# Kernel tuning notes

Measured on AMD Instinct MI355X. Metric: run time of the kernel, lower is better.

## Reference

```python
import jax, jax.numpy as jnp
import numpy as np

EPS = 0.0  # torch .norm division has no eps; keep exact

def setup_inputs() -> dict:
    key = jax.random.key(0)
    B, T, C = 32, 1024, 768
    x = jax.random.normal(key, (B, T, C), dtype=jnp.float32)
    return {"x": x}

def reference(x) -> jnp.ndarray:
    # Faithful device-side math of Block_ATC.forward -> agglomerative_clustering:
    #   metric = x / ||x||_2 (last dim); scores = metric @ metric^T; dist = 1 - scores
    # The subsequent scipy linkage/fcluster runs on CPU per-batch and its results
    # are discarded in the original code (labels stay zeros, forward returns None),
    # so the cosine-distance matrix is the meaningful computed tensor.
    metric = x / jnp.linalg.norm(x, axis=-1, keepdims=True)  # [B,T,C]
    scores = jnp.einsum('btc,bsc->bts', metric, metric)      # [B,T,T]
    return 1.0 - scores
```

## Files before the change

### kernel.cpp

```cpp
#include <hip/hip_runtime.h>
#include <hip/hip_bf16.h>
#include <stdint.h>
#include <math.h>

#define B_DIM 32
#define T_DIM 1024
#define C_DIM 768
#define NTILE 8
#define NTRI  36
#define KITER (C_DIM / 32)

typedef float f32x4 __attribute__((ext_vector_type(4)));

typedef __attribute__((address_space(1))) void gvoid_t;
typedef __attribute__((address_space(3))) void lvoid_t;

__global__ __launch_bounds__(256) void normalize_rows_fp8(const float* __restrict__ x,
                                                          uint32_t* __restrict__ m) {
    const int row  = blockIdx.x * 4 + (threadIdx.x >> 6);
    const int lane = threadIdx.x & 63;
    const float4* xr = (const float4*)(x + (size_t)row * C_DIM);
    float4 v0 = xr[lane];
    float4 v1 = xr[lane + 64];
    float4 v2 = xr[lane + 128];
    float ss = v0.x*v0.x + v0.y*v0.y + v0.z*v0.z + v0.w*v0.w
             + v1.x*v1.x + v1.y*v1.y + v1.z*v1.z + v1.w*v1.w
             + v2.x*v2.x + v2.y*v2.y + v2.z*v2.z + v2.w*v2.w;
    #pragma unroll
    for (int off = 32; off > 0; off >>= 1)
        ss += __shfl_xor(ss, off, 64);
    const float rs = rsqrtf(ss);
    uint32_t* mr = m + (size_t)row * (C_DIM / 4);
    int p;
    p = __builtin_amdgcn_cvt_pk_fp8_f32(v0.x * rs, v0.y * rs, 0, false);
    p = __builtin_amdgcn_cvt_pk_fp8_f32(v0.z * rs, v0.w * rs, p, true);
    mr[lane] = (uint32_t)p;
    p = __builtin_amdgcn_cvt_pk_fp8_f32(v1.x * rs, v1.y * rs, 0, false);
    p = __builtin_amdgcn_cvt_pk_fp8_f32(v1.z * rs, v1.w * rs, p, true);
    mr[lane + 64] = (uint32_t)p;
    p = __builtin_amdgcn_cvt_pk_fp8_f32(v2.x * rs, v2.y * rs, 0, false);
    p = __builtin_amdgcn_cvt_pk_fp8_f32(v2.z * rs, v2.w * rs, p, true);
    mr[lane + 128] = (uint32_t)p;
}

__global__ __launch_bounds__(256) void gemm_nt_sym_fp8(const uint8_t* __restrict__ M,
                                                       float* __restrict__ out) {
    __shared__ uint8_t As[2][128 * 32];
    __shared__ uint8_t Bs[2][128 * 32];

    const int b   = blockIdx.x & 31;
    const int idx = blockIdx.x >> 5;
    int tj = (int)((sqrtf(8.0f * (float)idx + 1.0f) - 1.0f) * 0.5f);
    if (tj * (tj + 1) / 2 > idx) --tj;
    const int ti = idx - tj * (tj + 1) / 2;

    const int tid  = threadIdx.x;
    const int wave = tid >> 6;
    const int lane = tid & 63;
    const int quad = lane >> 4;
    const int l16  = lane & 15;
    const int wi = wave >> 1;
    const int wj = wave & 1;

    const uint8_t* Mb = M + (size_t)b * T_DIM * C_DIM;

    const int srow = wave * 32 + (lane >> 1);
    const int scol = (lane & 1) * 16;

    const uint8_t* gA = Mb + (size_t)(ti * 128 + srow) * C_DIM + scol;
    const uint8_t* gB = Mb + (size_t)(tj * 128 + srow) * C_DIM + scol;
    const int cbase = wave * 1024;

    f32x4 acc[4][4];
    #pragma unroll
    for (int i = 0; i < 4; ++i)
        #pragma unroll
        for (int j = 0; j < 4; ++j)
            acc[i][j] = (f32x4){0.f, 0.f, 0.f, 0.f};

    __builtin_amdgcn_global_load_lds((gvoid_t*)gA, (lvoid_t*)&As[0][cbase], 16, 0, 0);
    __builtin_amdgcn_global_load_lds((gvoid_t*)gB, (lvoid_t*)&Bs[0][cbase], 16, 0, 0);

    for (int it = 0; it < KITER; ++it) {
        const int cur = it & 1;
        __syncthreads();
        if (it + 1 < KITER) {
            const int k0 = (it + 1) * 32;
            const int nxt = cur ^ 1;
            __builtin_amdgcn_global_load_lds((gvoid_t*)(gA + k0), (lvoid_t*)&As[nxt][cbase], 16, 0, 0);
            __builtin_amdgcn_global_load_lds((gvoid_t*)(gB + k0), (lvoid_t*)&Bs[nxt][cbase], 16, 0, 0);
        }

        long af[4], bfr[4];
        #pragma unroll
        for (int ii = 0; ii < 4; ++ii) {
            af[ii]  = *(const long*)&As[cur][(wi * 64 + ii * 16 + l16) * 32 + quad * 8];
            bfr[ii] = *(const long*)&Bs[cur][(wj * 64 + ii * 16 + l16) * 32 + quad * 8];
        }
        #pragma unroll
        for (int ii = 0; ii < 4; ++ii)
            #pragma unroll
            for (int jj = 0; jj < 4; ++jj)
                acc[ii][jj] = __builtin_amdgcn_mfma_f32_16x16x32_fp8_fp8(af[ii], bfr[jj], acc[ii][jj], 0, 0, 0);
    }

    float* outb = out + (size_t)b * T_DIM * T_DIM;
    #pragma unroll
    for (int ii = 0; ii < 4; ++ii) {
        const int rowbase = ti * 128 + wi * 64 + ii * 16 + quad * 4;
        #pragma unroll
        for (int jj = 0; jj < 4; ++jj) {
            const int col = tj * 128 + wj * 64 + jj * 16 + l16;
            #pragma unroll
            for (int r = 0; r < 4; ++r)
                outb[(size_t)(rowbase + r) * T_DIM + col] = 1.0f - acc[ii][jj][r];
        }
    }
    if (ti != tj) {
        #pragma unroll
        for (int ii = 0; ii < 4; ++ii) {
            const int rowbase = ti * 128 + wi * 64 + ii * 16 + quad * 4;
            #pragma unroll
            for (int jj = 0; jj < 4; ++jj) {
                const int col = tj * 128 + wj * 64 + jj * 16 + l16;
                f32x4 v;
                v[0] = 1.0f - acc[ii][jj][0];
                v[1] = 1.0f - acc[ii][jj][1];
                v[2] = 1.0f - acc[ii][jj][2];
                v[3] = 1.0f - acc[ii][jj][3];
                *(f32x4*)(outb + (size_t)col * T_DIM + rowbase) = v;
            }
        }
    }
}

extern "C" void kernel_launch(void* const* d_in, const int* in_sizes, int n_in,
                              void* d_out, int out_size, void* d_ws, size_t ws_size,
                              hipStream_t stream) {
    const float* x = (const float*)d_in[0];
    float* out = (float*)d_out;
    uint32_t* metric = (uint32_t*)d_ws;

    normalize_rows_fp8<<<dim3((B_DIM * T_DIM) / 4), dim3(256), 0, stream>>>(x, metric);
    gemm_nt_sym_fp8<<<dim3(NTRI * B_DIM), dim3(256), 0, stream>>>((const uint8_t*)metric, out);
}
```

Before: 250.3 us.

## Deepen LDS pipeline to four buffers with vmcnt waits and swizzle LDS layout

Expands the shared-memory staging from double to quad buffering with a prefetch distance of three K-steps. The full __syncthreads is replaced by explicit s_waitcnt vmcnt plus a raw barrier, so loads for later iterations can stay in flight. An XOR swizzle on the 16-byte column halves, keyed by row bit 2, is applied to both the global-to-LDS copy and the LDS fragment reads to reduce bank conflicts. The costs are more LDS per block (which may lower occupancy) and the risk that the hand-counted vmcnt values and the barrier placement leave a race between overwriting a buffer and other waves still reading it.

```diff
diff --git a/kernel.cpp b/kernel.cpp
--- a/kernel.cpp
+++ b/kernel.cpp
@@ -9,6 +9,7 @@
 #define NTILE 8
 #define NTRI  36
 #define KITER (C_DIM / 32)
+#define NBUF  4
 
 typedef float f32x4 __attribute__((ext_vector_type(4)));
 
@@ -45,8 +46,8 @@
 
 __global__ __launch_bounds__(256) void gemm_nt_sym_fp8(const uint8_t* __restrict__ M,
                                                        float* __restrict__ out) {
-    __shared__ uint8_t As[2][128 * 32];
-    __shared__ uint8_t Bs[2][128 * 32];
+    __shared__ uint8_t As[NBUF][128 * 32];
+    __shared__ uint8_t Bs[NBUF][128 * 32];
 
     const int b   = blockIdx.x & 31;
     const int idx = blockIdx.x >> 5;
@@ -65,11 +66,19 @@
     const uint8_t* Mb = M + (size_t)b * T_DIM * C_DIM;
 
     const int srow = wave * 32 + (lane >> 1);
-    const int scol = (lane & 1) * 16;
+    const int scol = ((lane & 1) * 16) ^ ((((srow >> 2) & 1)) << 4);
 
     const uint8_t* gA = Mb + (size_t)(ti * 128 + srow) * C_DIM + scol;
     const uint8_t* gB = Mb + (size_t)(tj * 128 + srow) * C_DIM + scol;
     const int cbase = wave * 1024;
+
+    const int sw = ((l16 >> 2) & 1) << 4;
+    int offA[4], offB[4];
+    #pragma unroll
+    for (int ii = 0; ii < 4; ++ii) {
+        offA[ii] = (wi * 64 + ii * 16 + l16) * 32 + ((quad * 8) ^ sw);
+        offB[ii] = (wj * 64 + ii * 16 + l16) * 32 + ((quad * 8) ^ sw);
+    }
 
     f32x4 acc[4][4];
     #pragma unroll
@@ -78,24 +87,37 @@
         for (int j = 0; j < 4; ++j)
             acc[i][j] = (f32x4){0.f, 0.f, 0.f, 0.f};
 
-    __builtin_amdgcn_global_load_lds((gvoid_t*)gA, (lvoid_t*)&As[0][cbase], 16, 0, 0);
-    __builtin_amdgcn_global_load_lds((gvoid_t*)gB, (lvoid_t*)&Bs[0][cbase], 16, 0, 0);
+    #pragma unroll
+    for (int pf = 0; pf < 3; ++pf) {
+        __builtin_amdgcn_global_load_lds((gvoid_t*)(gA + pf * 32), (lvoid_t*)&As[pf][cbase], 16, 0, 0);
+        __builtin_amdgcn_global_load_lds((gvoid_t*)(gB + pf * 32), (lvoid_t*)&Bs[pf][cbase], 16, 0, 0);
+    }
 
+    #pragma unroll 4
     for (int it = 0; it < KITER; ++it) {
-        const int cur = it & 1;
-        __syncthreads();
-        if (it + 1 < KITER) {
-            const int k0 = (it + 1) * 32;
-            const int nxt = cur ^ 1;
+        const int cur = it & (NBUF - 1);
+        if (it < KITER - 2) {
+            asm volatile("s_waitcnt vmcnt(4)" ::: "memory");
+        } else {
+            asm volatile("s_waitcnt vmcnt(0)" ::: "memory");
+        }
+        __builtin_amdgcn_s_barrier();
+        __builtin_amdgcn_sched_barrier(0);
+
+        if (it + 3 < KITER) {
+            const int k0 = (it + 3) * 32;
+            const int nxt = (it + 3) & (NBUF - 1);
             __builtin_amdgcn_global_load_lds((gvoid_t*)(gA + k0), (lvoid_t*)&As[nxt][cbase], 16, 0, 0);
             __builtin_amdgcn_global_load_lds((gvoid_t*)(gB + k0), (lvoid_t*)&Bs[nxt][cbase], 16, 0, 0);
         }
 
+        const uint8_t* a_base = &As[cur][0];
+        const uint8_t* b_base = &Bs[cur][0];
         long af[4], bfr[4];
         #pragma unroll
         for (int ii = 0; ii < 4; ++ii) {
-            af[ii]  = *(const long*)&As[cur][(wi * 64 + ii * 16 + l16) * 32 + quad * 8];
-            bfr[ii] = *(const long*)&Bs[cur][(wj * 64 + ii * 16 + l16) * 32 + quad * 8];
+            af[ii]  = *(const long*)(a_base + offA[ii]);
+            bfr[ii] = *(const long*)(b_base + offB[ii]);
         }
         #pragma unroll
         for (int ii = 0; ii < 4; ++ii)
```

Measured after the change: 256.1 us. 1.02x slower.

## Fuse row normalization into symmetric fp8 GEMM with epilogue scaling

Applied to the files above, without the earlier changes.

Removes the separate normalize pass and workspace by loading fp32 rows inside the GEMM, converting them to fp8 unnormalized, accumulating the squared norms alongside, and scaling by reciprocal norms in the epilogue. It also XOR-swizzles the LDS layout and uses nontemporal stores for both output triangles. The aim is to drop one launch and the fp8 intermediate round trip. In exchange, each tile re-reads fp32 rows (4x the bytes per reload), and the async global-to-LDS copy is replaced by register-staged prefetch with conversion work in the main loop.

```diff
diff --git a/kernel.cpp b/kernel.cpp
--- a/kernel.cpp
+++ b/kernel.cpp
@@ -1,5 +1,4 @@
 #include <hip/hip_runtime.h>
-#include <hip/hip_bf16.h>
 #include <stdint.h>
 #include <math.h>
 
@@ -11,42 +10,14 @@
 #define KITER (C_DIM / 32)
 
 typedef float f32x4 __attribute__((ext_vector_type(4)));
+typedef int   i32x4 __attribute__((ext_vector_type(4)));
 
-typedef __attribute__((address_space(1))) void gvoid_t;
-typedef __attribute__((address_space(3))) void lvoid_t;
-
-__global__ __launch_bounds__(256) void normalize_rows_fp8(const float* __restrict__ x,
-                                                          uint32_t* __restrict__ m) {
-    const int row  = blockIdx.x * 4 + (threadIdx.x >> 6);
-    const int lane = threadIdx.x & 63;
-    const float4* xr = (const float4*)(x + (size_t)row * C_DIM);
-    float4 v0 = xr[lane];
-    float4 v1 = xr[lane + 64];
-    float4 v2 = xr[lane + 128];
-    float ss = v0.x*v0.x + v0.y*v0.y + v0.z*v0.z + v0.w*v0.w
-             + v1.x*v1.x + v1.y*v1.y + v1.z*v1.z + v1.w*v1.w
-             + v2.x*v2.x + v2.y*v2.y + v2.z*v2.z + v2.w*v2.w;
-    #pragma unroll
-    for (int off = 32; off > 0; off >>= 1)
-        ss += __shfl_xor(ss, off, 64);
-    const float rs = rsqrtf(ss);
-    uint32_t* mr = m + (size_t)row * (C_DIM / 4);
-    int p;
-    p = __builtin_amdgcn_cvt_pk_fp8_f32(v0.x * rs, v0.y * rs, 0, false);
-    p = __builtin_amdgcn_cvt_pk_fp8_f32(v0.z * rs, v0.w * rs, p, true);
-    mr[lane] = (uint32_t)p;
-    p = __builtin_amdgcn_cvt_pk_fp8_f32(v1.x * rs, v1.y * rs, 0, false);
-    p = __builtin_amdgcn_cvt_pk_fp8_f32(v1.z * rs, v1.w * rs, p, true);
-    mr[lane + 64] = (uint32_t)p;
-    p = __builtin_amdgcn_cvt_pk_fp8_f32(v2.x * rs, v2.y * rs, 0, false);
-    p = __builtin_amdgcn_cvt_pk_fp8_f32(v2.z * rs, v2.w * rs, p, true);
-    mr[lane + 128] = (uint32_t)p;
-}
-
-__global__ __launch_bounds__(256) void gemm_nt_sym_fp8(const uint8_t* __restrict__ M,
-                                                       float* __restrict__ out) {
+__global__ __launch_bounds__(256) void fused_cosdist_fp8(const float* __restrict__ x,
+                                                         float* __restrict__ out) {
     __shared__ uint8_t As[2][128 * 32];
     __shared__ uint8_t Bs[2][128 * 32];
+    __shared__ float rsA[128];
+    __shared__ float rsB[128];
 
     const int b   = blockIdx.x & 31;
     const int idx = blockIdx.x >> 5;
@@ -55,21 +26,27 @@
     const int ti = idx - tj * (tj + 1) / 2;
 
     const int tid  = threadIdx.x;
+    const int lane = tid & 63;
     const int wave = tid >> 6;
-    const int lane = tid & 63;
     const int quad = lane >> 4;
     const int l16  = lane & 15;
     const int wi = wave >> 1;
     const int wj = wave & 1;
 
-    const uint8_t* Mb = M + (size_t)b * T_DIM * C_DIM;
+    const int r = tid >> 1;
+    const int h = tid & 1;
+    const float* xb = x + (size_t)b * T_DIM * C_DIM;
+    const float* gA = xb + (size_t)(ti * 128 + r) * C_DIM + h * 16;
+    const float* gB = xb + (size_t)(tj * 128 + r) * C_DIM + h * 16;
+    const int wbyte = r * 32 + ((h * 16) ^ (((r >> 2) & 1) << 4));
 
-    const int srow = wave * 32 + (lane >> 1);
-    const int scol = (lane & 1) * 16;
-
-    const uint8_t* gA = Mb + (size_t)(ti * 128 + srow) * C_DIM + scol;
-    const uint8_t* gB = Mb + (size_t)(tj * 128 + srow) * C_DIM + scol;
-    const int cbase = wave * 1024;
+    const int sw = ((l16 >> 2) & 1) << 4;
+    int offA[4], offB[4];
+    #pragma unroll
+    for (int ii = 0; ii < 4; ++ii) {
+        offA[ii] = (wi * 64 + ii * 16 + l16) * 32 + ((quad * 8) ^ sw);
+        offB[ii] = (wj * 64 + ii * 16 + l16) * 32 + ((quad * 8) ^ sw);
+    }
 
     f32x4 acc[4][4];
     #pragma unroll
@@ -78,60 +55,88 @@
         for (int j = 0; j < 4; ++j)
             acc[i][j] = (f32x4){0.f, 0.f, 0.f, 0.f};
 
-    __builtin_amdgcn_global_load_lds((gvoid_t*)gA, (lvoid_t*)&As[0][cbase], 16, 0, 0);
-    __builtin_amdgcn_global_load_lds((gvoid_t*)gB, (lvoid_t*)&Bs[0][cbase], 16, 0, 0);
+    float ssA = 0.f, ssB = 0.f;
+
+#define SS4(v) ((v).x*(v).x + (v).y*(v).y + (v).z*(v).z + (v).w*(v).w)
+#define CVT4(v) ({ int _t = __builtin_amdgcn_cvt_pk_fp8_f32((v).x, (v).y, 0, false); \
+                   __builtin_amdgcn_cvt_pk_fp8_f32((v).z, (v).w, _t, true); })
+
+    {
+        const float4* pA = (const float4*)gA;
+        const float4* pB = (const float4*)gB;
+        float4 a0 = pA[0], a1 = pA[1], a2 = pA[2], a3 = pA[3];
+        float4 b0 = pB[0], b1 = pB[1], b2 = pB[2], b3 = pB[3];
+        ssA += SS4(a0) + SS4(a1) + SS4(a2) + SS4(a3);
+        ssB += SS4(b0) + SS4(b1) + SS4(b2) + SS4(b3);
+        *(i32x4*)&As[0][wbyte] = (i32x4){CVT4(a0), CVT4(a1), CVT4(a2), CVT4(a3)};
+        *(i32x4*)&Bs[0][wbyte] = (i32x4){CVT4(b0), CVT4(b1), CVT4(b2), CVT4(b3)};
+    }
+    __syncthreads();
 
     for (int it = 0; it < KITER; ++it) {
         const int cur = it & 1;
-        __syncthreads();
-        if (it + 1 < KITER) {
-            const int k0 = (it + 1) * 32;
-            const int nxt = cur ^ 1;
-            __builtin_amdgcn_global_load_lds((gvoid_t*)(gA + k0), (lvoid_t*)&As[nxt][cbase], 16, 0, 0);
-            __builtin_amdgcn_global_load_lds((gvoid_t*)(gB + k0), (lvoid_t*)&Bs[nxt][cbase], 16, 0, 0);
+        const bool more = (it + 1 < KITER);
+
+        float4 na0, na1, na2, na3, nb0, nb1, nb2, nb3;
+        if (more) {
+            const float4* pA = (const float4*)(gA + (it + 1) * 32);
+            const float4* pB = (const float4*)(gB + (it + 1) * 32);
+            na0 = pA[0]; na1 = pA[1]; na2 = pA[2]; na3 = pA[3];
+            nb0 = pB[0]; nb1 = pB[1]; nb2 = pB[2]; nb3 = pB[3];
         }
 
         long af[4], bfr[4];
         #pragma unroll
         for (int ii = 0; ii < 4; ++ii) {
-            af[ii]  = *(const long*)&As[cur][(wi * 64 + ii * 16 + l16) * 32 + quad * 8];
-            bfr[ii] = *(const long*)&Bs[cur][(wj * 64 + ii * 16 + l16) * 32 + quad * 8];
+            af[ii]  = *(const long*)(&As[cur][0] + offA[ii]);
+            bfr[ii] = *(const long*)(&Bs[cur][0] + offB[ii]);
         }
         #pragma unroll
         for (int ii = 0; ii < 4; ++ii)
             #pragma unroll
             for (int jj = 0; jj < 4; ++jj)
                 acc[ii][jj] = __builtin_amdgcn_mfma_f32_16x16x32_fp8_fp8(af[ii], bfr[jj], acc[ii][jj], 0, 0, 0);
+
+        if (more) {
+            ssA += SS4(na0) + SS4(na1) + SS4(na2) + SS4(na3);
+            ssB += SS4(nb0) + SS4(nb1) + SS4(nb2) + SS4(nb3);
+            *(i32x4*)&As[cur ^ 1][wbyte] = (i32x4){CVT4(na0), CVT4(na1), CVT4(na2), CVT4(na3)};
+            *(i32x4*)&Bs[cur ^ 1][wbyte] = (i32x4){CVT4(nb0), CVT4(nb1), CVT4(nb2), CVT4(nb3)};
+        }
+        __syncthreads();
     }
+
+    ssA += __shfl_xor(ssA, 1, 64);
+    ssB += __shfl_xor(ssB, 1, 64);
+    rsA[r] = rsqrtf(ssA);
+    rsB[r] = rsqrtf(ssB);
+    __syncthreads();
 
     float* outb = out + (size_t)b * T_DIM * T_DIM;
     #pragma unroll
     for (int ii = 0; ii < 4; ++ii) {
-        const int rowbase = ti * 128 + wi * 64 + ii * 16 + quad * 4;
+        const int rl = wi * 64 + ii * 16 + quad * 4;
+        const f32x4 ra = *(const f32x4*)&rsA[rl];
+        const int rowbase = ti * 128 + rl;
         #pragma unroll
         for (int jj = 0; jj < 4; ++jj) {
-            const int col = tj * 128 + wj * 64 + jj * 16 + l16;
+            const int cl  = wj * 64 + jj * 16 + l16;
+            const float rb = rsB[cl];
+            const int col = tj * 128 + cl;
+            f32x4 v;
             #pragma unroll
-            for (int r = 0; r < 4; ++r)
-                outb[(size_t)(rowbase + r) * T_DIM + col] = 1.0f - acc[ii][jj][r];
-        }
-    }
-    if (ti != tj) {
-        #pragma unroll
-        for (int ii = 0; ii < 4; ++ii) {
-            const int rowbase = ti * 128 + wi * 64 + ii * 16 + quad * 4;
+            for (int rr = 0; rr < 4; ++rr)
+                v[rr] = 1.0f - acc[ii][jj][rr] * (ra[rr] * rb);
             #pragma unroll
-            for (int jj = 0; jj < 4; ++jj) {
-                const int col = tj * 128 + wj * 64 + jj * 16 + l16;
-                f32x4 v;
-                v[0] = 1.0f - acc[ii][jj][0];
-                v[1] = 1.0f - acc[ii][jj][1];
-                v[2] = 1.0f - acc[ii][jj][2];
-                v[3] = 1.0f - acc[ii][jj][3];
-                *(f32x4*)(outb + (size_t)col * T_DIM + rowbase) = v;
+            for (int rr = 0; rr < 4; ++rr)
+                __builtin_nontemporal_store(v[rr], &outb[(size_t)(rowbase + rr) * T_DIM + col]);
+            if (ti != tj) {
+                __builtin_nontemporal_store(v, (f32x4*)(outb + (size_t)col * T_DIM + rowbase));
             }
         }
     }
+#undef SS4
+#undef CVT4
 }
 
 extern "C" void kernel_launch(void* const* d_in, const int* in_sizes, int n_in,
@@ -139,8 +144,6 @@
                               hipStream_t stream) {
     const float* x = (const float*)d_in[0];
     float* out = (float*)d_out;
-    uint32_t* metric = (uint32_t*)d_ws;
-
-    normalize_rows_fp8<<<dim3((B_DIM * T_DIM) / 4), dim3(256), 0, stream>>>(x, metric);
-    gemm_nt_sym_fp8<<<dim3(NTRI * B_DIM), dim3(256), 0, stream>>>((const uint8_t*)metric, out);
+    (void)d_ws; (void)ws_size;
+    fused_cosdist_fp8<<<dim3(NTRI * B_DIM), dim3(256), 0, stream>>>(x, out);
 }
```

After: 295.0 us. 1.18x slower.

## Give each wave its own 64x64 triangular tile with private LDS pipeline

Applied to the files above, without the earlier changes.

Reworks the symmetric GEMM so each wave independently computes one 64x64 upper-triangle tile. Each wave stages its own A/B slices into private LDS and uses vmcnt waits in place of block-wide __syncthreads. It also adds an XOR swizzle on the LDS layout to reduce bank conflicts. Finer tiles waste less work on the diagonal and remove cross-wave synchronization, but operand reuse drops from 128-row to 64-row tiles, increasing global traffic per flop.

```diff
diff --git a/kernel.cpp b/kernel.cpp
--- a/kernel.cpp
+++ b/kernel.cpp
@@ -1,13 +1,14 @@
 #include <hip/hip_runtime.h>
-#include <hip/hip_bf16.h>
 #include <stdint.h>
 #include <math.h>
 
 #define B_DIM 32
 #define T_DIM 1024
 #define C_DIM 768
-#define NTILE 8
-#define NTRI  36
+#define WT    64
+#define NT    (T_DIM / WT)
+#define NTRI  (NT * (NT + 1) / 2)
+#define NBLK  (NTRI / 4)
 #define KITER (C_DIM / 32)
 
 typedef float f32x4 __attribute__((ext_vector_type(4)));
@@ -43,33 +44,44 @@
     mr[lane + 128] = (uint32_t)p;
 }
 
-__global__ __launch_bounds__(256) void gemm_nt_sym_fp8(const uint8_t* __restrict__ M,
-                                                       float* __restrict__ out) {
-    __shared__ uint8_t As[2][128 * 32];
-    __shared__ uint8_t Bs[2][128 * 32];
+__global__ __launch_bounds__(256) void gemm_nt_sym_fp8_wave(const uint8_t* __restrict__ M,
+                                                            float* __restrict__ out) {
+    __shared__ uint8_t lds[4][2][2][WT * 32];
 
-    const int b   = blockIdx.x & 31;
-    const int idx = blockIdx.x >> 5;
-    int tj = (int)((sqrtf(8.0f * (float)idx + 1.0f) - 1.0f) * 0.5f);
-    if (tj * (tj + 1) / 2 > idx) --tj;
-    const int ti = idx - tj * (tj + 1) / 2;
-
+    const int b  = blockIdx.x & 31;
+    const int tg = blockIdx.x >> 5;
     const int tid  = threadIdx.x;
     const int wave = tid >> 6;
     const int lane = tid & 63;
     const int quad = lane >> 4;
     const int l16  = lane & 15;
-    const int wi = wave >> 1;
-    const int wj = wave & 1;
+
+    const int t = tg * 4 + wave;
+    int tj = (int)((sqrtf(8.0f * (float)t + 1.0f) - 1.0f) * 0.5f);
+    if (tj * (tj + 1) / 2 > t) --tj;
+    if ((tj + 1) * (tj + 2) / 2 <= t) ++tj;
+    const int ti = t - tj * (tj + 1) / 2;
 
     const uint8_t* Mb = M + (size_t)b * T_DIM * C_DIM;
 
-    const int srow = wave * 32 + (lane >> 1);
-    const int scol = (lane & 1) * 16;
+    const int srow = lane >> 1;
+    const int scol = ((lane & 1) * 16) ^ (((lane >> 3) & 1) << 4);
+    const uint8_t* gA = Mb + (size_t)(ti * WT + srow) * C_DIM + scol;
+    const uint8_t* gB = Mb + (size_t)(tj * WT + srow) * C_DIM + scol;
 
-    const uint8_t* gA = Mb + (size_t)(ti * 128 + srow) * C_DIM + scol;
-    const uint8_t* gB = Mb + (size_t)(tj * 128 + srow) * C_DIM + scol;
-    const int cbase = wave * 1024;
+#define STAGE(buf_, koff_)                                                                                   \
+    do {                                                                                                     \
+        __builtin_amdgcn_global_load_lds((gvoid_t*)(gA + (koff_)),               (lvoid_t*)&lds[wave][buf_][0][0],    16, 0, 0); \
+        __builtin_amdgcn_global_load_lds((gvoid_t*)(gA + (koff_) + 32 * C_DIM),  (lvoid_t*)&lds[wave][buf_][0][1024], 16, 0, 0); \
+        __builtin_amdgcn_global_load_lds((gvoid_t*)(gB + (koff_)),               (lvoid_t*)&lds[wave][buf_][1][0],    16, 0, 0); \
+        __builtin_amdgcn_global_load_lds((gvoid_t*)(gB + (koff_) + 32 * C_DIM),  (lvoid_t*)&lds[wave][buf_][1][1024], 16, 0, 0); \
+    } while (0)
+
+    const int sw = ((l16 >> 2) & 1) << 4;
+    int offF[4];
+    #pragma unroll
+    for (int ii = 0; ii < 4; ++ii)
+        offF[ii] = (ii * 16 + l16) * 32 + ((quad * 8) ^ sw);
 
     f32x4 acc[4][4];
     #pragma unroll
@@ -78,24 +90,24 @@
         for (int j = 0; j < 4; ++j)
             acc[i][j] = (f32x4){0.f, 0.f, 0.f, 0.f};
 
-    __builtin_amdgcn_global_load_lds((gvoid_t*)gA, (lvoid_t*)&As[0][cbase], 16, 0, 0);
-    __builtin_amdgcn_global_load_lds((gvoid_t*)gB, (lvoid_t*)&Bs[0][cbase], 16, 0, 0);
+    STAGE(0, 0);
 
     for (int it = 0; it < KITER; ++it) {
         const int cur = it & 1;
-        __syncthreads();
+        __builtin_amdgcn_sched_barrier(0);
         if (it + 1 < KITER) {
-            const int k0 = (it + 1) * 32;
-            const int nxt = cur ^ 1;
-            __builtin_amdgcn_global_load_lds((gvoid_t*)(gA + k0), (lvoid_t*)&As[nxt][cbase], 16, 0, 0);
-            __builtin_amdgcn_global_load_lds((gvoid_t*)(gB + k0), (lvoid_t*)&Bs[nxt][cbase], 16, 0, 0);
+            STAGE(cur ^ 1, (it + 1) * 32);
+            asm volatile("s_waitcnt vmcnt(4)" ::: "memory");
+        } else {
+            asm volatile("s_waitcnt vmcnt(0)" ::: "memory");
         }
+        __builtin_amdgcn_sched_barrier(0);
 
         long af[4], bfr[4];
         #pragma unroll
         for (int ii = 0; ii < 4; ++ii) {
-            af[ii]  = *(const long*)&As[cur][(wi * 64 + ii * 16 + l16) * 32 + quad * 8];
-            bfr[ii] = *(const long*)&Bs[cur][(wj * 64 + ii * 16 + l16) * 32 + quad * 8];
+            af[ii]  = *(const long*)&lds[wave][cur][0][offF[ii]];
+            bfr[ii] = *(const long*)&lds[wave][cur][1][offF[ii]];
         }
         #pragma unroll
         for (int ii = 0; ii < 4; ++ii)
@@ -103,14 +115,15 @@
             for (int jj = 0; jj < 4; ++jj)
                 acc[ii][jj] = __builtin_amdgcn_mfma_f32_16x16x32_fp8_fp8(af[ii], bfr[jj], acc[ii][jj], 0, 0, 0);
     }
+#undef STAGE
 
     float* outb = out + (size_t)b * T_DIM * T_DIM;
     #pragma unroll
     for (int ii = 0; ii < 4; ++ii) {
-        const int rowbase = ti * 128 + wi * 64 + ii * 16 + quad * 4;
+        const int rowbase = ti * WT + ii * 16 + quad * 4;
         #pragma unroll
         for (int jj = 0; jj < 4; ++jj) {
-            const int col = tj * 128 + wj * 64 + jj * 16 + l16;
+            const int col = tj * WT + jj * 16 + l16;
             #pragma unroll
             for (int r = 0; r < 4; ++r)
                 outb[(size_t)(rowbase + r) * T_DIM + col] = 1.0f - acc[ii][jj][r];
@@ -119,10 +132,10 @@
     if (ti != tj) {
         #pragma unroll
         for (int ii = 0; ii < 4; ++ii) {
-            const int rowbase = ti * 128 + wi * 64 + ii * 16 + quad * 4;
+            const int rowbase = ti * WT + ii * 16 + quad * 4;
             #pragma unroll
             for (int jj = 0; jj < 4; ++jj) {
-                const int col = tj * 128 + wj * 64 + jj * 16 + l16;
+                const int col = tj * WT + jj * 16 + l16;
                 f32x4 v;
                 v[0] = 1.0f - acc[ii][jj][0];
                 v[1] = 1.0f - acc[ii][jj][1];
@@ -142,5 +155,5 @@
     uint32_t* metric = (uint32_t*)d_ws;
 
     normalize_rows_fp8<<<dim3((B_DIM * T_DIM) / 4), dim3(256), 0, stream>>>(x, metric);
-    gemm_nt_sym_fp8<<<dim3(NTRI * B_DIM), dim3(256), 0, stream>>>((const uint8_t*)metric, out);
+    gemm_nt_sym_fp8_wave<<<dim3(NBLK * B_DIM), dim3(256), 0, stream>>>((const uint8_t*)metric, out);
 }
```

Measured after the change: 258.6 us. 1.03x slower.
